# Optimization experiments

Hardware: AMD Instinct MI355X
Metric: run time of the kernel (lower is better)

The kernel has to match this reference:

```python
import jax, jax.numpy as jnp
import numpy as np

BS, N, C, KNN = 2, 65536, 256, 16

def setup_inputs() -> dict:
    key = jax.random.key(0)
    ks = jax.random.split(key, 8)
    s = 1.0 / np.sqrt(C)
    return {
        "Q": jax.random.normal(ks[0], (BS, N, C), jnp.float32),
        "K": jax.random.normal(ks[1], (BS, N, C), jnp.float32),
        "V": jax.random.normal(ks[2], (BS, N, C), jnp.float32),
        "knn_idx": jax.random.randint(ks[3], (N, KNN), 0, N, jnp.int32),
        "Wq_w": jax.random.normal(ks[4], (C, C), jnp.float32) * s,
        "Wq_b": jnp.zeros((C,), jnp.float32),
        "Wk_w": jax.random.normal(ks[5], (C, C), jnp.float32) * s,
        "Wk_b": jnp.zeros((C,), jnp.float32),
        "Wv_w": jax.random.normal(ks[6], (C, C), jnp.float32) * s,
        "Wv_b": jnp.zeros((C,), jnp.float32),
        "ln_g": jnp.ones((C,), jnp.float32),
        "ln_b": jnp.zeros((C,), jnp.float32),
    }

def _layernorm(x, g, b, eps=1e-5):
    mu = jnp.mean(x, axis=-1, keepdims=True)
    var = jnp.mean(jnp.square(x - mu), axis=-1, keepdims=True)
    return (x - mu) * jax.lax.rsqrt(var + eps) * g + b

def reference(Q, K, V, knn_idx, Wq_w, Wq_b, Wk_w, Wk_b, Wv_w, Wv_b, ln_g, ln_b):
    c = Q.shape[-1]
    # torch nn.Linear: x @ W.T + b
    Qp = Q @ Wq_w.T + Wq_b                     # (bs, N, C)
    Kp = K @ Wk_w.T + Wk_b
    Vp = V @ Wv_w.T + Wv_b
    K_knn = Kp[:, knn_idx, :]                  # (bs, N, k, C) gather over node dim
    V_knn = Vp[:, knn_idx, :]
    attn = jnp.einsum('bnc,bnkc->bnk', Qp, K_knn) / jnp.sqrt(jnp.asarray(c, Qp.dtype))
    attn = jax.nn.softmax(attn, axis=-1)       # (bs, N, k)
    out = jnp.einsum('bnk,bnkc->bnc', attn, V_knn)
    return _layernorm(out + Qp, ln_g, ln_b)
```

## Files before the change

### kernel.cpp

```cpp
#include <hip/hip_runtime.h>

#define BS 2
#define NN 65536
#define CC 256
#define KNNK 16

typedef short bf16x8 __attribute__((ext_vector_type(8)));
typedef float f32x4 __attribute__((ext_vector_type(4)));

__device__ __forceinline__ unsigned f2bf(float f) {
  unsigned u = __builtin_bit_cast(unsigned, f);
  return (u + 0x7FFFu + ((u >> 16) & 1u)) >> 16;
}
__device__ __forceinline__ int pack2(float a, float b) {
  return (int)(f2bf(a) | (f2bf(b) << 16));
}
__device__ __forceinline__ float bfu(unsigned short v) {
  return __builtin_bit_cast(float, ((unsigned)v) << 16);
}
__device__ __forceinline__ float bflo(unsigned u) { return __builtin_bit_cast(float, u << 16); }
__device__ __forceinline__ float bfhi(unsigned u) { return __builtin_bit_cast(float, u & 0xFFFF0000u); }

template <int OUT_BF16>
__global__ __launch_bounds__(512)
void proj_kernel(const float* __restrict__ A, const float* __restrict__ W,
                 const float* __restrict__ bias, void* __restrict__ Out) {
  constexpr int K = 256, TM = 128, LDS_S = 40;
  __shared__ __align__(16) unsigned short As[TM * LDS_S];
  __shared__ __align__(16) unsigned short Bs[256 * LDS_S];
  const int t = threadIdx.x;
  const int wave = t >> 6;
  const int lane = t & 63;
  const int wm = wave >> 2, wn = wave & 3;
  const int lrow = lane & 15, quad = lane >> 4;
  const long row0 = (long)blockIdx.x * TM;

  const int ar = t >> 2, akb = t & 3;
  const int br = t >> 1, bkb = t & 1;
  const float* aptr = A + (row0 + ar) * K + akb * 8;
  const float* bptr = W + (long)br * K + bkb * 16;

  f32x4 acc[4][4];
#pragma unroll
  for (int i = 0; i < 4; ++i)
#pragma unroll
    for (int j = 0; j < 4; ++j) acc[i][j] = f32x4{0.f, 0.f, 0.f, 0.f};

  for (int k0 = 0; k0 < K; k0 += 32) {
    float4 a0 = *(const float4*)(aptr + k0);
    float4 a1 = *(const float4*)(aptr + k0 + 4);
    float4 b0 = *(const float4*)(bptr + k0);
    float4 b1 = *(const float4*)(bptr + k0 + 4);
    float4 b2 = *(const float4*)(bptr + k0 + 8);
    float4 b3 = *(const float4*)(bptr + k0 + 12);
    __syncthreads();
    *(int4*)&As[ar * LDS_S + akb * 8] =
        make_int4(pack2(a0.x, a0.y), pack2(a0.z, a0.w), pack2(a1.x, a1.y), pack2(a1.z, a1.w));
    *(int4*)&Bs[br * LDS_S + bkb * 16] =
        make_int4(pack2(b0.x, b0.y), pack2(b0.z, b0.w), pack2(b1.x, b1.y), pack2(b1.z, b1.w));
    *(int4*)&Bs[br * LDS_S + bkb * 16 + 8] =
        make_int4(pack2(b2.x, b2.y), pack2(b2.z, b2.w), pack2(b3.x, b3.y), pack2(b3.z, b3.w));
    __syncthreads();
    bf16x8 af[4], bfr[4];
#pragma unroll
    for (int mi = 0; mi < 4; ++mi)
      af[mi] = *(const bf16x8*)&As[(wm * 64 + mi * 16 + lrow) * LDS_S + quad * 8];
#pragma unroll
    for (int ni = 0; ni < 4; ++ni)
      bfr[ni] = *(const bf16x8*)&Bs[(wn * 64 + ni * 16 + lrow) * LDS_S + quad * 8];
#pragma unroll
    for (int mi = 0; mi < 4; ++mi)
#pragma unroll
      for (int ni = 0; ni < 4; ++ni)
        acc[mi][ni] = __builtin_amdgcn_mfma_f32_16x16x32_bf16(af[mi], bfr[ni], acc[mi][ni], 0, 0, 0);
  }

#pragma unroll
  for (int mi = 0; mi < 4; ++mi)
#pragma unroll
    for (int ni = 0; ni < 4; ++ni) {
      const long gr0 = row0 + wm * 64 + mi * 16 + quad * 4;
      const int gc = wn * 64 + ni * 16 + lrow;
      const float bv = bias[gc];
#pragma unroll
      for (int r = 0; r < 4; ++r) {
        float v = acc[mi][ni][r] + bv;
        if (OUT_BF16)
          ((unsigned short*)Out)[(gr0 + r) * 256 + gc] = (unsigned short)f2bf(v);
        else
          ((float*)Out)[(gr0 + r) * 256 + gc] = v;
      }
    }
}

__global__ __launch_bounds__(256)
void attn_kernel(const float* __restrict__ Qp, const unsigned short* __restrict__ Kp,
                 const unsigned short* __restrict__ Vp, const int* __restrict__ knn,
                 const float* __restrict__ ln_g, const float* __restrict__ ln_b,
                 float* __restrict__ out) {
  const int n = blockIdx.x, b = blockIdx.y, t = threadIdx.x;
  __shared__ int sidx[KNNK];
  __shared__ float sdots[KNNK];
  __shared__ float sred[8];
  if (t < KNNK) sidx[t] = knn[n * KNNK + t];
  __syncthreads();

  const long base = ((long)b * NN + n) * CC;
  const long kbase = (long)b * NN * CC;
  int nbr[KNNK];
#pragma unroll
  for (int i = 0; i < KNNK; ++i) nbr[i] = sidx[i];

  const int k = t >> 4, cg = t & 15;
  {
    const float* qp = Qp + base + cg * 16;
    float4 q0 = *(const float4*)(qp);
    float4 q1 = *(const float4*)(qp + 4);
    float4 q2 = *(const float4*)(qp + 8);
    float4 q3 = *(const float4*)(qp + 12);
    const unsigned short* kr = Kp + kbase + (long)nbr[k] * CC + cg * 16;
    int4 kv0 = *(const int4*)(kr);
    int4 kv1 = *(const int4*)(kr + 8);
    float p = q0.x * bflo(kv0.x) + q0.y * bfhi(kv0.x)
            + q0.z * bflo(kv0.y) + q0.w * bfhi(kv0.y)
            + q1.x * bflo(kv0.z) + q1.y * bfhi(kv0.z)
            + q1.z * bflo(kv0.w) + q1.w * bfhi(kv0.w)
            + q2.x * bflo(kv1.x) + q2.y * bfhi(kv1.x)
            + q2.z * bflo(kv1.y) + q2.w * bfhi(kv1.y)
            + q3.x * bflo(kv1.z) + q3.y * bfhi(kv1.z)
            + q3.z * bflo(kv1.w) + q3.w * bfhi(kv1.w);
#pragma unroll
    for (int m = 1; m < 16; m <<= 1) p += __shfl_xor(p, m);
    if (cg == 0) sdots[k] = p * 0.0625f;
  }
  __syncthreads();

  float d[KNNK];
#pragma unroll
  for (int i = 0; i < KNNK; ++i) d[i] = sdots[i];
  float mx = d[0];
#pragma unroll
  for (int i = 1; i < KNNK; ++i) mx = fmaxf(mx, d[i]);
  float s = 0.f;
#pragma unroll
  for (int i = 0; i < KNNK; ++i) { d[i] = __expf(d[i] - mx); s += d[i]; }
  const float inv = 1.0f / s;

  float o = 0.f;
#pragma unroll
  for (int i = 0; i < KNNK; ++i)
    o += d[i] * bfu(Vp[kbase + (long)nbr[i] * CC + t]);
  o *= inv;
  o += Qp[base + t];

  float s1 = o, s2 = o * o;
#pragma unroll
  for (int m = 1; m < 64; m <<= 1) {
    s1 += __shfl_xor(s1, m);
    s2 += __shfl_xor(s2, m);
  }
  const int wv = t >> 6;
  if ((t & 63) == 0) { sred[wv] = s1; sred[wv + 4] = s2; }
  __syncthreads();
  const float S1 = sred[0] + sred[1] + sred[2] + sred[3];
  const float S2 = sred[4] + sred[5] + sred[6] + sred[7];
  const float mu = S1 * (1.0f / 256.0f);
  const float var = S2 * (1.0f / 256.0f) - mu * mu;
  const float rs = rsqrtf(var + 1e-5f);
  out[base + t] = (o - mu) * rs * ln_g[t] + ln_b[t];
}

extern "C" void kernel_launch(void* const* d_in, const int* in_sizes, int n_in,
                              void* d_out, int out_size, void* d_ws, size_t ws_size,
                              hipStream_t stream) {
  const float* Q   = (const float*)d_in[0];
  const float* K   = (const float*)d_in[1];
  const float* V   = (const float*)d_in[2];
  const int*   knn = (const int*)d_in[3];
  const float* Wq  = (const float*)d_in[4];
  const float* Wqb = (const float*)d_in[5];
  const float* Wk  = (const float*)d_in[6];
  const float* Wkb = (const float*)d_in[7];
  const float* Wv  = (const float*)d_in[8];
  const float* Wvb = (const float*)d_in[9];
  const float* ln_g = (const float*)d_in[10];
  const float* ln_b = (const float*)d_in[11];
  float* out = (float*)d_out;

  float* Qp = (float*)d_ws;
  unsigned short* Kp = (unsigned short*)((char*)d_ws + (size_t)BS * NN * CC * 4);
  unsigned short* Vp = Kp + (size_t)BS * NN * CC;

  proj_kernel<0><<<1024, 512, 0, stream>>>(Q, Wq, Wqb, (void*)Qp);
  proj_kernel<1><<<1024, 512, 0, stream>>>(K, Wk, Wkb, (void*)Kp);
  proj_kernel<1><<<1024, 512, 0, stream>>>(V, Wv, Wvb, (void*)Vp);
  attn_kernel<<<dim3(NN, BS), 256, 0, stream>>>(Qp, Kp, Vp, knn, ln_g, ln_b, out);
}
```

Baseline: 795.5 us.

## Store Qp as bf16, pre-convert weights, and map one wave per node in attention

Weights are converted to bf16 once in a small prep kernel, so each projection block no longer reloads and converts fp32 weights. Qp is now stored in bf16, which halves its write and read traffic. The attention kernel is restructured so each wave handles one node: dot products, softmax and LayerNorm are all done with wave shuffles and readlane, with no LDS or block barriers. It also uses vectorized V gathers and output stores. The costs are lower precision for Qp and the residual term, plus round-half-up bf16 rounding in place of round-to-nearest-even.

```diff
diff --git a/kernel.cpp b/kernel.cpp
--- a/kernel.cpp
+++ b/kernel.cpp
@@ -8,23 +8,33 @@
 typedef short bf16x8 __attribute__((ext_vector_type(8)));
 typedef float f32x4 __attribute__((ext_vector_type(4)));
 
-__device__ __forceinline__ unsigned f2bf(float f) {
-  unsigned u = __builtin_bit_cast(unsigned, f);
-  return (u + 0x7FFFu + ((u >> 16) & 1u)) >> 16;
-}
-__device__ __forceinline__ int pack2(float a, float b) {
-  return (int)(f2bf(a) | (f2bf(b) << 16));
-}
-__device__ __forceinline__ float bfu(unsigned short v) {
-  return __builtin_bit_cast(float, ((unsigned)v) << 16);
+__device__ __forceinline__ unsigned pk_rnd(float a, float b) {
+  unsigned ua = __builtin_bit_cast(unsigned, a) + 0x8000u;
+  unsigned ub = __builtin_bit_cast(unsigned, b) + 0x8000u;
+  return __builtin_amdgcn_perm(ub, ua, 0x07060302u);
+}
+__device__ __forceinline__ unsigned short f2bf1(float f) {
+  return (unsigned short)((__builtin_bit_cast(unsigned, f) + 0x8000u) >> 16);
 }
 __device__ __forceinline__ float bflo(unsigned u) { return __builtin_bit_cast(float, u << 16); }
 __device__ __forceinline__ float bfhi(unsigned u) { return __builtin_bit_cast(float, u & 0xFFFF0000u); }
 
-template <int OUT_BF16>
+__global__ __launch_bounds__(256)
+void prep_w(const float* __restrict__ W0, const float* __restrict__ W1,
+            const float* __restrict__ W2, unsigned short* __restrict__ D0,
+            unsigned short* __restrict__ D1, unsigned short* __restrict__ D2) {
+  const float* src = (blockIdx.y == 0) ? W0 : (blockIdx.y == 1) ? W1 : W2;
+  unsigned short* dst = (blockIdx.y == 0) ? D0 : (blockIdx.y == 1) ? D1 : D2;
+  const int i = (blockIdx.x * 256 + threadIdx.x) * 8;
+  float4 a = *(const float4*)(src + i);
+  float4 b = *(const float4*)(src + i + 4);
+  *(int4*)(dst + i) = make_int4(pk_rnd(a.x, a.y), pk_rnd(a.z, a.w),
+                                pk_rnd(b.x, b.y), pk_rnd(b.z, b.w));
+}
+
 __global__ __launch_bounds__(512)
-void proj_kernel(const float* __restrict__ A, const float* __restrict__ W,
-                 const float* __restrict__ bias, void* __restrict__ Out) {
+void proj_kernel(const float* __restrict__ A, const unsigned short* __restrict__ Wb,
+                 const float* __restrict__ bias, unsigned short* __restrict__ Out) {
   constexpr int K = 256, TM = 128, LDS_S = 40;
   __shared__ __align__(16) unsigned short As[TM * LDS_S];
   __shared__ __align__(16) unsigned short Bs[256 * LDS_S];
@@ -38,7 +48,7 @@
   const int ar = t >> 2, akb = t & 3;
   const int br = t >> 1, bkb = t & 1;
   const float* aptr = A + (row0 + ar) * K + akb * 8;
-  const float* bptr = W + (long)br * K + bkb * 16;
+  const unsigned short* bptr = Wb + (long)br * K + bkb * 16;
 
   f32x4 acc[4][4];
 #pragma unroll
@@ -49,17 +59,13 @@
   for (int k0 = 0; k0 < K; k0 += 32) {
     float4 a0 = *(const float4*)(aptr + k0);
     float4 a1 = *(const float4*)(aptr + k0 + 4);
-    float4 b0 = *(const float4*)(bptr + k0);
-    float4 b1 = *(const float4*)(bptr + k0 + 4);
-    float4 b2 = *(const float4*)(bptr + k0 + 8);
-    float4 b3 = *(const float4*)(bptr + k0 + 12);
+    int4 b0 = *(const int4*)(bptr + k0);
+    int4 b1 = *(const int4*)(bptr + k0 + 8);
     __syncthreads();
     *(int4*)&As[ar * LDS_S + akb * 8] =
-        make_int4(pack2(a0.x, a0.y), pack2(a0.z, a0.w), pack2(a1.x, a1.y), pack2(a1.z, a1.w));
-    *(int4*)&Bs[br * LDS_S + bkb * 16] =
-        make_int4(pack2(b0.x, b0.y), pack2(b0.z, b0.w), pack2(b1.x, b1.y), pack2(b1.z, b1.w));
-    *(int4*)&Bs[br * LDS_S + bkb * 16 + 8] =
-        make_int4(pack2(b2.x, b2.y), pack2(b2.z, b2.w), pack2(b3.x, b3.y), pack2(b3.z, b3.w));
+        make_int4(pk_rnd(a0.x, a0.y), pk_rnd(a0.z, a0.w), pk_rnd(a1.x, a1.y), pk_rnd(a1.z, a1.w));
+    *(int4*)&Bs[br * LDS_S + bkb * 16] = b0;
+    *(int4*)&Bs[br * LDS_S + bkb * 16 + 8] = b1;
     __syncthreads();
     bf16x8 af[4], bfr[4];
 #pragma unroll
@@ -83,91 +89,87 @@
       const int gc = wn * 64 + ni * 16 + lrow;
       const float bv = bias[gc];
 #pragma unroll
-      for (int r = 0; r < 4; ++r) {
-        float v = acc[mi][ni][r] + bv;
-        if (OUT_BF16)
-          ((unsigned short*)Out)[(gr0 + r) * 256 + gc] = (unsigned short)f2bf(v);
-        else
-          ((float*)Out)[(gr0 + r) * 256 + gc] = v;
-      }
+      for (int r = 0; r < 4; ++r)
+        Out[(gr0 + r) * 256 + gc] = f2bf1(acc[mi][ni][r] + bv);
     }
 }
 
 __global__ __launch_bounds__(256)
-void attn_kernel(const float* __restrict__ Qp, const unsigned short* __restrict__ Kp,
+void attn_kernel(const unsigned short* __restrict__ Qp, const unsigned short* __restrict__ Kp,
                  const unsigned short* __restrict__ Vp, const int* __restrict__ knn,
                  const float* __restrict__ ln_g, const float* __restrict__ ln_b,
                  float* __restrict__ out) {
-  const int n = blockIdx.x, b = blockIdx.y, t = threadIdx.x;
-  __shared__ int sidx[KNNK];
-  __shared__ float sdots[KNNK];
-  __shared__ float sred[8];
-  if (t < KNNK) sidx[t] = knn[n * KNNK + t];
-  __syncthreads();
-
+  const int lane = threadIdx.x & 63;
+  const int wv = threadIdx.x >> 6;
+  const int n = blockIdx.x * 4 + wv;
+  const int b = blockIdx.y;
   const long base = ((long)b * NN + n) * CC;
   const long kbase = (long)b * NN * CC;
-  int nbr[KNNK];
-#pragma unroll
-  for (int i = 0; i < KNNK; ++i) nbr[i] = sidx[i];
-
-  const int k = t >> 4, cg = t & 15;
-  {
-    const float* qp = Qp + base + cg * 16;
-    float4 q0 = *(const float4*)(qp);
-    float4 q1 = *(const float4*)(qp + 4);
-    float4 q2 = *(const float4*)(qp + 8);
-    float4 q3 = *(const float4*)(qp + 12);
-    const unsigned short* kr = Kp + kbase + (long)nbr[k] * CC + cg * 16;
-    int4 kv0 = *(const int4*)(kr);
-    int4 kv1 = *(const int4*)(kr + 8);
-    float p = q0.x * bflo(kv0.x) + q0.y * bfhi(kv0.x)
-            + q0.z * bflo(kv0.y) + q0.w * bfhi(kv0.y)
-            + q1.x * bflo(kv0.z) + q1.y * bfhi(kv0.z)
-            + q1.z * bflo(kv0.w) + q1.w * bfhi(kv0.w)
-            + q2.x * bflo(kv1.x) + q2.y * bfhi(kv1.x)
-            + q2.z * bflo(kv1.y) + q2.w * bfhi(kv1.y)
-            + q3.x * bflo(kv1.z) + q3.y * bfhi(kv1.z)
-            + q3.z * bflo(kv1.w) + q3.w * bfhi(kv1.w);
-#pragma unroll
-    for (int m = 1; m < 16; m <<= 1) p += __shfl_xor(p, m);
-    if (cg == 0) sdots[k] = p * 0.0625f;
-  }
-  __syncthreads();
-
-  float d[KNNK];
-#pragma unroll
-  for (int i = 0; i < KNNK; ++i) d[i] = sdots[i];
-  float mx = d[0];
-#pragma unroll
-  for (int i = 1; i < KNNK; ++i) mx = fmaxf(mx, d[i]);
-  float s = 0.f;
-#pragma unroll
-  for (int i = 0; i < KNNK; ++i) { d[i] = __expf(d[i] - mx); s += d[i]; }
-  const float inv = 1.0f / s;
-
-  float o = 0.f;
-#pragma unroll
-  for (int i = 0; i < KNNK; ++i)
-    o += d[i] * bfu(Vp[kbase + (long)nbr[i] * CC + t]);
-  o *= inv;
-  o += Qp[base + t];
-
-  float s1 = o, s2 = o * o;
+
+  const int k = lane & 15, q = lane >> 4;
+  const int nbr = knn[n * KNNK + k];
+
+  const int4* krow = (const int4*)(Kp + kbase + (long)nbr * CC + q * 64);
+  const int4* qrow = (const int4*)(Qp + base + q * 64);
+  float acc0 = 0.f, acc1 = 0.f;
+#pragma unroll
+  for (int j = 0; j < 8; ++j) {
+    int4 kv = krow[j];
+    int4 qv = qrow[j];
+    acc0 += bflo(kv.x) * bflo(qv.x) + bfhi(kv.x) * bfhi(qv.x);
+    acc1 += bflo(kv.y) * bflo(qv.y) + bfhi(kv.y) * bfhi(qv.y);
+    acc0 += bflo(kv.z) * bflo(qv.z) + bfhi(kv.z) * bfhi(qv.z);
+    acc1 += bflo(kv.w) * bflo(qv.w) + bfhi(kv.w) * bfhi(qv.w);
+  }
+  float dot = acc0 + acc1;
+  dot += __shfl_xor(dot, 16);
+  dot += __shfl_xor(dot, 32);
+  dot *= 0.0625f;
+
+  float mx = dot;
+#pragma unroll
+  for (int m = 1; m < 16; m <<= 1) mx = fmaxf(mx, __shfl_xor(mx, m));
+  float e = __expf(dot - mx);
+  float s = e;
+#pragma unroll
+  for (int m = 1; m < 16; m <<= 1) s += __shfl_xor(s, m);
+  const float w = e / s;
+
+  float o0 = 0.f, o1 = 0.f, o2 = 0.f, o3 = 0.f;
+  const unsigned short* Vb = Vp + kbase;
+#pragma unroll
+  for (int k2 = 0; k2 < KNNK; ++k2) {
+    const int nb = __builtin_amdgcn_readlane(nbr, k2);
+    const float wk = __builtin_bit_cast(float,
+        __builtin_amdgcn_readlane(__builtin_bit_cast(int, w), k2));
+    const unsigned short* row = Vb + (long)nb * CC;
+    int2 vv = *(const int2*)(row + lane * 4);
+    o0 += wk * bflo(vv.x); o1 += wk * bfhi(vv.x);
+    o2 += wk * bflo(vv.y); o3 += wk * bfhi(vv.y);
+  }
+
+  int2 qres = *(const int2*)(Qp + base + lane * 4);
+  o0 += bflo(qres.x); o1 += bfhi(qres.x);
+  o2 += bflo(qres.y); o3 += bfhi(qres.y);
+
+  float s1 = o0 + o1 + o2 + o3;
+  float s2 = o0 * o0 + o1 * o1 + o2 * o2 + o3 * o3;
 #pragma unroll
   for (int m = 1; m < 64; m <<= 1) {
     s1 += __shfl_xor(s1, m);
     s2 += __shfl_xor(s2, m);
   }
-  const int wv = t >> 6;
-  if ((t & 63) == 0) { sred[wv] = s1; sred[wv + 4] = s2; }
-  __syncthreads();
-  const float S1 = sred[0] + sred[1] + sred[2] + sred[3];
-  const float S2 = sred[4] + sred[5] + sred[6] + sred[7];
-  const float mu = S1 * (1.0f / 256.0f);
-  const float var = S2 * (1.0f / 256.0f) - mu * mu;
+  const float mu = s1 * (1.0f / 256.0f);
+  const float var = s2 * (1.0f / 256.0f) - mu * mu;
   const float rs = rsqrtf(var + 1e-5f);
-  out[base + t] = (o - mu) * rs * ln_g[t] + ln_b[t];
+  float4 g = *(const float4*)(ln_g + lane * 4);
+  float4 bv = *(const float4*)(ln_b + lane * 4);
+  float4 res;
+  res.x = (o0 - mu) * rs * g.x + bv.x;
+  res.y = (o1 - mu) * rs * g.y + bv.y;
+  res.z = (o2 - mu) * rs * g.z + bv.z;
+  res.w = (o3 - mu) * rs * g.w + bv.w;
+  *(float4*)(out + base + lane * 4) = res;
 }
 
 extern "C" void kernel_launch(void* const* d_in, const int* in_sizes, int n_in,
@@ -187,12 +189,17 @@
   const float* ln_b = (const float*)d_in[11];
   float* out = (float*)d_out;
 
-  float* Qp = (float*)d_ws;
-  unsigned short* Kp = (unsigned short*)((char*)d_ws + (size_t)BS * NN * CC * 4);
-  unsigned short* Vp = Kp + (size_t)BS * NN * CC;
-
-  proj_kernel<0><<<1024, 512, 0, stream>>>(Q, Wq, Wqb, (void*)Qp);
-  proj_kernel<1><<<1024, 512, 0, stream>>>(K, Wk, Wkb, (void*)Kp);
-  proj_kernel<1><<<1024, 512, 0, stream>>>(V, Wv, Wvb, (void*)Vp);
-  attn_kernel<<<dim3(NN, BS), 256, 0, stream>>>(Qp, Kp, Vp, knn, ln_g, ln_b, out);
-}
+  const size_t NE = (size_t)BS * NN * CC;
+  unsigned short* Qp = (unsigned short*)d_ws;
+  unsigned short* Kp = Qp + NE;
+  unsigned short* Vp = Kp + NE;
+  unsigned short* Wqb16 = Vp + NE;
+  unsigned short* Wkb16 = Wqb16 + CC * CC;
+  unsigned short* Wvb16 = Wkb16 + CC * CC;
+
+  prep_w<<<dim3(32, 3), 256, 0, stream>>>(Wq, Wk, Wv, Wqb16, Wkb16, Wvb16);
+  proj_kernel<<<1024, 512, 0, stream>>>(Q, Wqb16, Wqb, Qp);
+  proj_kernel<<<1024, 512, 0, stream>>>(K, Wkb16, Wkb, Kp);
+  proj_kernel<<<1024, 512, 0, stream>>>(V, Wvb16, Wvb, Vp);
+  attn_kernel<<<dim3(NN / 4, BS), 256, 0, stream>>>(Qp, Kp, Vp, knn, ln_g, ln_b, out);
+}
```

Result: no change. 800.3 us (+0.6%).
